# Optimization experiments

Hardware: AMD Instinct MI355X
Metric: run time of the kernel (lower is better)

## Reference

```python
import jax, jax.numpy as jnp
import numpy as np

B, S, D = 4, 512, 256

def setup_inputs() -> dict:
    key = jax.random.key(0)
    ks = jax.random.split(key, 32)
    def w(k, shape, s=0.05):
        return jax.random.normal(k, shape, dtype=jnp.float32) * s
    inp = {
        "img": jax.random.normal(ks[0], (B, S, D), dtype=jnp.float32),
        "audio": jax.random.normal(ks[1], (B, S, D), dtype=jnp.float32),
        "common": jax.random.normal(ks[2], (B, S, D), dtype=jnp.float32),
    }
    names = ["qv", "qa", "kv", "ka", "cc", "w5", "w6", "w7", "w8"]
    for i, n in enumerate(names):
        inp[n + "_w"] = w(ks[3 + 2 * i], (D, D))   # stored [in, out]
        inp[n + "_b"] = w(ks[4 + 2 * i], (D,))
    inp["bil_w"] = w(ks[25], (D, D, D))            # Bilinear weight [out, in1, in2]
    inp["t_o"] = jnp.ones((), dtype=jnp.float32)
    return inp


def reference(img, audio, common,
              qv_w, qv_b, qa_w, qa_b, kv_w, kv_b, ka_w, ka_b, cc_w, cc_b,
              w5_w, w5_b, w6_w, w6_b, w7_w, w7_b, w8_w, w8_b,
              bil_w, t_o):
    dim_k = qv_w.shape[1]
    norm_fact = 1.0 / jnp.sqrt(jnp.asarray(dim_k, dtype=jnp.float32))

    lin = lambda x, w, b: x @ w + b
    # NOTE: faithful to source - softmax first, THEN scaled by norm_fact.
    attn = lambda q, k: jax.nn.softmax(jnp.einsum('bsd,btd->bst', q, k), axis=-1) * norm_fact

    W_q_v = lin(img, qv_w, qv_b)
    W_q_a = lin(audio, qa_w, qa_b)
    w_k_a = lin(audio, ka_w, ka_b)
    W_k_v = lin(img, kv_w, kv_b)
    C_c = lin(common, cc_w, cc_b)

    atten_vv = attn(W_q_v, W_k_v)
    atten_vc = attn(W_q_v, C_c)
    atten_aa = attn(W_q_a, w_k_a)
    atten_ac = attn(W_q_a, C_c)

    vc_common = jnp.einsum('bst,btd->bsd', atten_vc, common)
    ac_common = jnp.einsum('bst,btd->bsd', atten_ac, common)

    common_feat_v = (1.0 + lin(vc_common, w5_w, w5_b)) * jnp.einsum('bst,btd->bsd', atten_vv, img) + lin(vc_common, w6_w, w6_b)
    common_feat_a = (1.0 + lin(ac_common, w7_w, w7_b)) * jnp.einsum('bst,btd->bsd', atten_aa, audio) + lin(ac_common, w8_w, w8_b)

    # Bilinear: out[b,s,k] = v[b,s,:] @ W[k] @ a[b,s,:]
    atten_m = jnp.einsum('bsi,kij,bsj->bsk', common_feat_v, bil_w, common_feat_a)
    j_o = jax.nn.sigmoid(atten_m)
    Z_k_o = t_o * j_o * img + (1.0 - j_o) * audio
    return (Z_k_o + img, Z_k_o + audio)
```

## Files before the change

kernel.cpp:

```cpp
#include <hip/hip_runtime.h>
#include <hip/hip_bf16.h>

typedef unsigned short ushortT;
typedef __bf16 bf16x8 __attribute__((ext_vector_type(8)));
typedef float f32x4 __attribute__((ext_vector_type(4)));
typedef ushortT ush8 __attribute__((ext_vector_type(8)));
typedef ushortT ush4 __attribute__((ext_vector_type(4)));

#define MFMA16(a, b, c) __builtin_amdgcn_mfma_f32_16x16x32_bf16((a), (b), (c), 0, 0, 0)

__device__ __forceinline__ ushortT f2b(float f) {
  __hip_bfloat16 h = __float2bfloat16(f);
  return __builtin_bit_cast(ushortT, h);
}
__device__ __forceinline__ float b2f(ushortT u) {
  __hip_bfloat16 h = __builtin_bit_cast(__hip_bfloat16, u);
  return __bfloat162float(h);
}

__device__ __forceinline__ void async16(const void* g, void* l) {
  __builtin_amdgcn_global_load_lds((const __attribute__((address_space(1))) unsigned int*)g,
                                   (__attribute__((address_space(3))) unsigned int*)l, 16, 0, 0);
}

#define ACT_E 524288
#define WD_E  65536

#define OFF_ACT16   0u
#define OFF_ACTT16  3145728u
#define OFF_W16T    6291456u
#define OFF_PROJ16  7471104u
#define OFF_P16     12713984u
#define OFF_VC16    21102592u
#define OFF_AC16    22151168u
#define OFF_PVV32   23199744u
#define OFF_PVA32   25296896u
#define OFF_PART    0u
#define OFF_BIL16   33554432u
#define OFF_CFV16   67108864u
#define OFF_CFA16   68157440u

__global__ void k_cvt_acts(const float* __restrict__ img, const float* __restrict__ aud,
                           const float* __restrict__ com, ushortT* __restrict__ dst) {
  int i4 = blockIdx.x * 256 + threadIdx.x;
#pragma unroll
  for (int q = 0; q < 4; q++) {
    int idx4 = i4 + q * 98304;
    int flat = idx4 * 4;
    const float* src;
    int off;
    if (flat < 524288)        { src = img; off = flat; }
    else if (flat < 1048576)  { src = aud; off = flat - 524288; }
    else                      { src = com; off = flat - 1048576; }
    float4 v = *(const float4*)(src + off);
    ush4 u = { f2b(v.x), f2b(v.y), f2b(v.z), f2b(v.w) };
    *(ush4*)(dst + idx4 * 4) = u;
  }
}

__global__ void k_cvt_bil(const float* __restrict__ bil, ushortT* __restrict__ dst) {
  int i4 = blockIdx.x * 256 + threadIdx.x;
#pragma unroll
  for (int q = 0; q < 8; q++) {
    int idx4 = i4 + q * 524288;
    float4 v = *(const float4*)(bil + idx4 * 4);
    ush4 u = { f2b(v.x), f2b(v.y), f2b(v.z), f2b(v.w) };
    *(ush4*)(dst + idx4 * 4) = u;
  }
}

__global__ void k_transpose(const float* __restrict__ img, const float* __restrict__ aud,
                            const float* __restrict__ com,
                            const float* w0, const float* w1, const float* w2,
                            const float* w3, const float* w4, const float* w5,
                            const float* w6, const float* w7, const float* w8,
                            ushortT* __restrict__ actT, ushortT* __restrict__ wT) {
  __shared__ ushortT tl[64][72];
  int tid = threadIdx.x;
  int bx = blockIdx.x;
  const float* src;
  ushortT* dst;
  int R, C, r0, c0;
  if (bx < 384) {
    int inst = bx >> 5, tile = bx & 31;
    int act = inst >> 2, bb = inst & 3;
    src = (act == 0 ? img : (act == 1 ? aud : com)) + bb * 131072;
    dst = actT + act * 524288 + bb * 131072;
    R = 512; C = 256;
    r0 = (tile >> 2) * 64; c0 = (tile & 3) * 64;
  } else {
    int bw = bx - 384;
    int w = bw >> 4, tile = bw & 15;
    const float* s;
    switch (w) {
      case 0: s = w0; break; case 1: s = w1; break; case 2: s = w2; break;
      case 3: s = w3; break; case 4: s = w4; break; case 5: s = w5; break;
      case 6: s = w6; break; case 7: s = w7; break; default: s = w8; break;
    }
    src = s;
    dst = wT + w * 65536;
    R = 256; C = 256;
    r0 = (tile >> 2) * 64; c0 = (tile & 3) * 64;
  }
#pragma unroll
  for (int q = 0; q < 4; q++) {
    int rr = q * 16 + (tid >> 4);
    int cs = (tid & 15) * 4;
    float4 v = *(const float4*)(src + (r0 + rr) * C + c0 + cs);
    tl[rr][cs + 0] = f2b(v.x);
    tl[rr][cs + 1] = f2b(v.y);
    tl[rr][cs + 2] = f2b(v.z);
    tl[rr][cs + 3] = f2b(v.w);
  }
  __syncthreads();
#pragma unroll
  for (int q = 0; q < 4; q++) {
    int cc = q * 16 + (tid >> 4);
    int rs = (tid & 15) * 4;
    ush4 u = { tl[rs + 0][cc], tl[rs + 1][cc], tl[rs + 2][cc], tl[rs + 3][cc] };
    *(ush4*)(dst + (c0 + cc) * R + r0 + rs) = u;
  }
}

__global__ __launch_bounds__(512) void k_linear5(
    const ushortT* __restrict__ act16, const ushortT* __restrict__ wT,
    const float* __restrict__ b0, const float* __restrict__ b1,
    const float* __restrict__ b2, const float* __restrict__ b3,
    const float* __restrict__ b4, ushortT* __restrict__ proj16) {
  __shared__ ushortT Al[4][32][8];
  __shared__ ushortT Bl[4][256][8];
  const int tid = threadIdx.x, l = tid & 63, w = tid >> 6;
  const int bx = blockIdx.x;
  const int op = bx >> 6, sblk = bx & 63;
  const int s0 = sblk * 32;
  const int xsel = (op == 4) ? 2 : (op & 1);
  const ushortT* X = act16 + xsel * ACT_E;
  const ushortT* W = wT + op * WD_E;
  const float* bias = op == 0 ? b0 : op == 1 ? b1 : op == 2 ? b2 : op == 3 ? b3 : b4;
  ushortT* out = proj16 + op * ACT_E;

  f32x4 acc[2][2] = {};
  ush8 ra, rb[2];
  int a_row = tid >> 2, a_seg = tid & 3;

  auto sload = [&](int k0) {
    if (tid < 128) ra = *(const ush8*)(X + (s0 + a_row) * 256 + k0 + a_seg * 8);
#pragma unroll
    for (int q = 0; q < 2; q++) {
      int slot = tid + q * 512;
      rb[q] = *(const ush8*)(W + (slot >> 2) * 256 + k0 + (slot & 3) * 8);
    }
  };
  auto swrite = [&]() {
    if (tid < 128) *(ush8*)(&Al[a_seg][a_row][0]) = ra;
#pragma unroll
    for (int q = 0; q < 2; q++) {
      int slot = tid + q * 512;
      *(ush8*)(&Bl[slot & 3][slot >> 2][0]) = rb[q];
    }
  };

  sload(0); swrite(); __syncthreads();
  for (int s = 0; s < 8; s++) {
    if (s < 7) sload((s + 1) * 32);
    int ks = l >> 4;
    bf16x8 a[2], bb[2];
#pragma unroll
    for (int m = 0; m < 2; m++) a[m] = *(const bf16x8*)(&Al[ks][m * 16 + (l & 15)][0]);
#pragma unroll
    for (int n = 0; n < 2; n++) bb[n] = *(const bf16x8*)(&Bl[ks][w * 32 + n * 16 + (l & 15)][0]);
#pragma unroll
    for (int m = 0; m < 2; m++)
#pragma unroll
      for (int n = 0; n < 2; n++) acc[m][n] = MFMA16(a[m], bb[n], acc[m][n]);
    if (s == 7) break;
    __syncthreads();
    swrite();
    __syncthreads();
  }
#pragma unroll
  for (int m = 0; m < 2; m++)
#pragma unroll
    for (int n = 0; n < 2; n++)
#pragma unroll
      for (int r = 0; r < 4; r++) {
        int row = s0 + m * 16 + (l >> 4) * 4 + r;
        int col = w * 32 + n * 16 + (l & 15);
        out[row * 256 + col] = f2b(acc[m][n][r] + bias[col]);
      }
}

__global__ __launch_bounds__(512) void k_attn(const ushortT* __restrict__ proj16,
                                              ushortT* __restrict__ P16) {
  __shared__ ushortT Ql[8][4][32][8];
  __shared__ ushortT Kl[4][512][8];
  __shared__ float red[32][8];
  const int tid = threadIdx.x, l = tid & 63, w = tid >> 6;
  const int bx = blockIdx.x;
  const int p = bx >> 6, b = (bx >> 4) & 3, sblk = bx & 15;
  const int s0 = sblk * 32;
  const int qsel = (p < 2) ? 0 : 1;
  const int ksel = (p == 0) ? 2 : (p == 2) ? 3 : 4;
  const ushortT* Q = proj16 + qsel * ACT_E + b * 131072;
  const ushortT* K = proj16 + ksel * ACT_E + b * 131072;
  ushortT* P = P16 + p * 1048576 + b * 262144;

#pragma unroll
  for (int q = 0; q < 2; q++) {
    int slot = tid + q * 512;
    int row = slot >> 5, seg = slot & 31;
    ush8 v = *(const ush8*)(Q + (s0 + row) * 256 + seg * 8);
    *(ush8*)(&Ql[seg >> 2][seg & 3][row][0]) = v;
  }

  f32x4 acc[2][4] = {};
  ush8 rk[4];
  auto kload = [&](int d0) {
#pragma unroll
    for (int q = 0; q < 4; q++) {
      int slot = tid + q * 512;
      rk[q] = *(const ush8*)(K + (slot >> 2) * 256 + d0 + (slot & 3) * 8);
    }
  };
  auto kwrite = [&]() {
#pragma unroll
    for (int q = 0; q < 4; q++) {
      int slot = tid + q * 512;
      *(ush8*)(&Kl[slot & 3][slot >> 2][0]) = rk[q];
    }
  };

  kload(0); kwrite(); __syncthreads();
  for (int s = 0; s < 8; s++) {
    if (s < 7) kload((s + 1) * 32);
    int ks = l >> 4;
    bf16x8 a[2], bb[4];
#pragma unroll
    for (int m = 0; m < 2; m++) a[m] = *(const bf16x8*)(&Ql[s][ks][m * 16 + (l & 15)][0]);
#pragma unroll
    for (int n = 0; n < 4; n++) bb[n] = *(const bf16x8*)(&Kl[ks][w * 64 + n * 16 + (l & 15)][0]);
#pragma unroll
    for (int m = 0; m < 2; m++)
#pragma unroll
      for (int n = 0; n < 4; n++) acc[m][n] = MFMA16(a[m], bb[n], acc[m][n]);
    if (s == 7) break;
    __syncthreads();
    kwrite();
    __syncthreads();
  }

  float gmax[2][4];
#pragma unroll
  for (int m = 0; m < 2; m++)
#pragma unroll
    for (int r = 0; r < 4; r++) {
      float v = fmaxf(fmaxf(acc[m][0][r], acc[m][1][r]), fmaxf(acc[m][2][r], acc[m][3][r]));
#pragma unroll
      for (int off = 1; off < 16; off <<= 1) v = fmaxf(v, __shfl_xor(v, off, 16));
      if ((l & 15) == 0) red[m * 16 + (l >> 4) * 4 + r][w] = v;
    }
  __syncthreads();
#pragma unroll
  for (int m = 0; m < 2; m++)
#pragma unroll
    for (int r = 0; r < 4; r++) {
      int sr = m * 16 + (l >> 4) * 4 + r;
      float g = red[sr][0];
#pragma unroll
      for (int ww = 1; ww < 8; ww++) g = fmaxf(g, red[sr][ww]);
      gmax[m][r] = g;
    }
  __syncthreads();
#pragma unroll
  for (int m = 0; m < 2; m++)
#pragma unroll
    for (int r = 0; r < 4; r++) {
      float ssum = 0.f;
#pragma unroll
      for (int n = 0; n < 4; n++) {
        float e = __expf(acc[m][n][r] - gmax[m][r]);
        acc[m][n][r] = e;
        ssum += e;
      }
#pragma unroll
      for (int off = 1; off < 16; off <<= 1) ssum += __shfl_xor(ssum, off, 16);
      if ((l & 15) == 0) red[m * 16 + (l >> 4) * 4 + r][w] = ssum;
    }
  __syncthreads();
#pragma unroll
  for (int m = 0; m < 2; m++)
#pragma unroll
    for (int r = 0; r < 4; r++) {
      int sr = m * 16 + (l >> 4) * 4 + r;
      float tot = 0.f;
#pragma unroll
      for (int ww = 0; ww < 8; ww++) tot += red[sr][ww];
      float sc = 0.0625f / tot;
#pragma unroll
      for (int n = 0; n < 4; n++)
        P[(s0 + sr) * 512 + w * 64 + n * 16 + (l & 15)] = f2b(acc[m][n][r] * sc);
    }
}

__global__ __launch_bounds__(512) void k_pv(const ushortT* __restrict__ P16,
                                            const ushortT* __restrict__ actT,
                                            float* __restrict__ pvv, float* __restrict__ pva,
                                            ushortT* __restrict__ vc16, ushortT* __restrict__ ac16) {
  __shared__ ushortT Al[4][32][8];
  __shared__ ushortT Bl[4][256][8];
  const int tid = threadIdx.x, l = tid & 63, w = tid >> 6;
  const int bx = blockIdx.x;
  const int p = bx >> 6, b = (bx >> 4) & 3, sblk = bx & 15;
  const int s0 = sblk * 32;
  const ushortT* A = P16 + p * 1048576 + b * 262144;
  const int vsel = (p == 0) ? 0 : (p == 2) ? 1 : 2;
  const ushortT* VT = actT + vsel * ACT_E + b * 131072;

  f32x4 acc[2][2] = {};
  ush8 ra, rb[2];
  int a_row = tid >> 2, a_seg = tid & 3;
  auto sload = [&](int t0) {
    if (tid < 128) ra = *(const ush8*)(A + (s0 + a_row) * 512 + t0 + a_seg * 8);
#pragma unroll
    for (int q = 0; q < 2; q++) {
      int slot = tid + q * 512;
      rb[q] = *(const ush8*)(VT + (slot >> 2) * 512 + t0 + (slot & 3) * 8);
    }
  };
  auto swrite = [&]() {
    if (tid < 128) *(ush8*)(&Al[a_seg][a_row][0]) = ra;
#pragma unroll
    for (int q = 0; q < 2; q++) {
      int slot = tid + q * 512;
      *(ush8*)(&Bl[slot & 3][slot >> 2][0]) = rb[q];
    }
  };

  sload(0); swrite(); __syncthreads();
  for (int s = 0; s < 16; s++) {
    if (s < 15) sload((s + 1) * 32);
    int ks = l >> 4;
    bf16x8 a[2], bb[2];
#pragma unroll
    for (int m = 0; m < 2; m++) a[m] = *(const bf16x8*)(&Al[ks][m * 16 + (l & 15)][0]);
#pragma unroll
    for (int n = 0; n < 2; n++) bb[n] = *(const bf16x8*)(&Bl[ks][w * 32 + n * 16 + (l & 15)][0]);
#pragma unroll
    for (int m = 0; m < 2; m++)
#pragma unroll
      for (int n = 0; n < 2; n++) acc[m][n] = MFMA16(a[m], bb[n], acc[m][n]);
    if (s == 15) break;
    __syncthreads();
    swrite();
    __syncthreads();
  }
#pragma unroll
  for (int m = 0; m < 2; m++)
#pragma unroll
    for (int n = 0; n < 2; n++)
#pragma unroll
      for (int r = 0; r < 4; r++) {
        int row = s0 + m * 16 + (l >> 4) * 4 + r;
        int col = w * 32 + n * 16 + (l & 15);
        int gi = (b * 512 + row) * 256 + col;
        float v = acc[m][n][r];
        if (p == 0) pvv[gi] = v;
        else if (p == 1) vc16[gi] = f2b(v);
        else if (p == 2) pva[gi] = v;
        else ac16[gi] = f2b(v);
      }
}

__global__ __launch_bounds__(512) void k_lin4c(
    const ushortT* __restrict__ vc16, const ushortT* __restrict__ ac16,
    const ushortT* __restrict__ wT,
    const float* __restrict__ w5b, const float* __restrict__ w6b,
    const float* __restrict__ w7b, const float* __restrict__ w8b,
    const float* __restrict__ pvv, const float* __restrict__ pva,
    ushortT* __restrict__ cfv, ushortT* __restrict__ cfa) {
  __shared__ ushortT Al[4][32][8];
  __shared__ ushortT B1[4][256][8];
  __shared__ ushortT B2[4][256][8];
  const int tid = threadIdx.x, l = tid & 63, w = tid >> 6;
  const int bx = blockIdx.x;
  const int side = bx >> 6, sblk = bx & 63;
  const int s0 = sblk * 32;
  const ushortT* A = side ? ac16 : vc16;
  const ushortT* W1 = wT + (side ? 7 : 5) * WD_E;
  const ushortT* W2 = wT + (side ? 8 : 6) * WD_E;
  const float* bb1 = side ? w7b : w5b;
  const float* bb2 = side ? w8b : w6b;
  const float* pv = side ? pva : pvv;
  ushortT* out = side ? cfa : cfv;

  f32x4 acc1[2][2] = {}, acc2[2][2] = {};
  ush8 ra, rb1[2], rb2[2];
  int a_row = tid >> 2, a_seg = tid & 3;
  auto sload = [&](int k0) {
    if (tid < 128) ra = *(const ush8*)(A + (s0 + a_row) * 256 + k0 + a_seg * 8);
#pragma unroll
    for (int q = 0; q < 2; q++) {
      int slot = tid + q * 512;
      rb1[q] = *(const ush8*)(W1 + (slot >> 2) * 256 + k0 + (slot & 3) * 8);
      rb2[q] = *(const ush8*)(W2 + (slot >> 2) * 256 + k0 + (slot & 3) * 8);
    }
  };
  auto swrite = [&]() {
    if (tid < 128) *(ush8*)(&Al[a_seg][a_row][0]) = ra;
#pragma unroll
    for (int q = 0; q < 2; q++) {
      int slot = tid + q * 512;
      *(ush8*)(&B1[slot & 3][slot >> 2][0]) = rb1[q];
      *(ush8*)(&B2[slot & 3][slot >> 2][0]) = rb2[q];
    }
  };

  sload(0); swrite(); __syncthreads();
  for (int s = 0; s < 8; s++) {
    if (s < 7) sload((s + 1) * 32);
    int ks = l >> 4;
    bf16x8 a[2], x1[2], x2[2];
#pragma unroll
    for (int m = 0; m < 2; m++) a[m] = *(const bf16x8*)(&Al[ks][m * 16 + (l & 15)][0]);
#pragma unroll
    for (int n = 0; n < 2; n++) {
      x1[n] = *(const bf16x8*)(&B1[ks][w * 32 + n * 16 + (l & 15)][0]);
      x2[n] = *(const bf16x8*)(&B2[ks][w * 32 + n * 16 + (l & 15)][0]);
    }
#pragma unroll
    for (int m = 0; m < 2; m++)
#pragma unroll
      for (int n = 0; n < 2; n++) {
        acc1[m][n] = MFMA16(a[m], x1[n], acc1[m][n]);
        acc2[m][n] = MFMA16(a[m], x2[n], acc2[m][n]);
      }
    if (s == 7) break;
    __syncthreads();
    swrite();
    __syncthreads();
  }
#pragma unroll
  for (int m = 0; m < 2; m++)
#pragma unroll
    for (int n = 0; n < 2; n++)
#pragma unroll
      for (int r = 0; r < 4; r++) {
        int row = s0 + m * 16 + (l >> 4) * 4 + r;
        int col = w * 32 + n * 16 + (l & 15);
        int gi = row * 256 + col;
        float u1 = acc1[m][n][r] + bb1[col];
        float u2 = acc2[m][n][r] + bb2[col];
        out[gi] = f2b((1.f + u1) * pv[gi] + u2);
      }
}

__global__ __launch_bounds__(256, 2) void k_bilinear3(
    const ushortT* __restrict__ cfa, const ushortT* __restrict__ cfv,
    const ushortT* __restrict__ W, float* __restrict__ part) {
  __shared__ char arena[57344];
  const int tid = threadIdx.x, l = tid & 63, w = tid >> 6;
  const int bx = blockIdx.x;
  const int ic = bx >> 5;
  const int mb = (bx >> 1) & 15;
  const int nb = bx & 1;
  const int r0 = mb * 128;
  const int ko0 = nb * 128;
  const int wr = w >> 1, wc = w & 1;

  float* cfvl = (float*)(arena + 49152);
  {
    int row = tid >> 1, seg = tid & 1;
    ush8 v = *(const ush8*)(cfv + (r0 + row) * 256 + ic * 16 + seg * 8);
    float* d = cfvl + row * 16 + seg * 8;
#pragma unroll
    for (int q = 0; q < 8; q++) d[q] = b2f(v[q]);
  }
  __syncthreads();

  int aP0 = tid * 16, aP1 = (tid + 256) * 16;
  int aL0 = aP0 ^ (((aP0 >> 7) & 7) << 4);
  int aL1 = aP1 ^ (((aP1 >> 7) & 7) << 4);
  const ushortT* gA0 = cfa + (r0 + (aL0 >> 6)) * 256 + ((aL0 >> 4) & 3) * 8;
  const ushortT* gA1 = cfa + (r0 + (aL1 >> 6)) * 256 + ((aL1 >> 4) & 3) * 8;
  const ushortT* gB0 = W + (ko0 + (aL0 >> 6)) * 65536 + ic * 4096 + ((aL0 >> 4) & 3) * 8;
  const ushortT* gB1 = W + (ko0 + (aL1 >> 6)) * 65536 + ic * 4096 + ((aL1 >> 4) & 3) * 8;

  int aoff[4], boff[4];
#pragma unroll
  for (int m = 0; m < 4; m++) {
    int row = wr * 64 + m * 16 + (l & 15);
    int byte = row * 64 + (l >> 4) * 16;
    aoff[m] = byte ^ (((byte >> 7) & 7) << 4);
  }
#pragma unroll
  for (int n = 0; n < 4; n++) {
    int row = wc * 64 + n * 16 + (l & 15);
    int byte = row * 64 + (l >> 4) * 16;
    boff[n] = byte ^ (((byte >> 7) & 7) << 4);
  }

  f32x4 macc[4][4] = {};
  f32x4 acci[4][4] = {};

  {
    char* Ab = arena;  char* Bb = arena + 24576;
    async16(gA0 + 0, Ab + aP0);  async16(gA1 + 0, Ab + aP1);
    async16(gB0 + 0, Bb + aP0);  async16(gB1 + 0, Bb + aP1);
    Ab += 8192; Bb += 8192;
    async16(gA0 + 32, Ab + aP0); async16(gA1 + 32, Ab + aP1);
    async16(gB0 + 32, Bb + aP0); async16(gB1 + 32, Bb + aP1);
  }

  int bi = 0, si = 2;
  for (int t = 0; t < 128; t++) {
    if (t < 126) asm volatile("s_waitcnt vmcnt(4)" ::: "memory");
    else         asm volatile("s_waitcnt vmcnt(0)" ::: "memory");
    __builtin_amdgcn_s_barrier();

    char* Ab = arena + bi * 8192;
    char* Bb = arena + 24576 + bi * 8192;
    bf16x8 af[4], bf[4];
#pragma unroll
    for (int m = 0; m < 4; m++) af[m] = *(const bf16x8*)(Ab + aoff[m]);
#pragma unroll
    for (int n = 0; n < 4; n++) bf[n] = *(const bf16x8*)(Bb + boff[n]);
#pragma unroll
    for (int m = 0; m < 4; m++)
#pragma unroll
      for (int n = 0; n < 4; n++) acci[m][n] = MFMA16(af[m], bf[n], acci[m][n]);

    if ((t & 7) == 7) {
      int il = t >> 3;
#pragma unroll
      for (int m = 0; m < 4; m++) {
        int rbase = wr * 64 + m * 16 + ((l >> 4) << 2);
        float c0 = cfvl[(rbase + 0) * 16 + il];
        float c1 = cfvl[(rbase + 1) * 16 + il];
        float c2 = cfvl[(rbase + 2) * 16 + il];
        float c3 = cfvl[(rbase + 3) * 16 + il];
#pragma unroll
        for (int n = 0; n < 4; n++) {
          macc[m][n][0] += c0 * acci[m][n][0];
          macc[m][n][1] += c1 * acci[m][n][1];
          macc[m][n][2] += c2 * acci[m][n][2];
          macc[m][n][3] += c3 * acci[m][n][3];
          acci[m][n] = (f32x4){0.f, 0.f, 0.f, 0.f};
        }
      }
    }

    if (t < 126) {
      char* An = arena + si * 8192;
      char* Bn = arena + 24576 + si * 8192;
      int ts = t + 2;
      int js = (ts & 7) * 32;
      async16(gA0 + js, An + aP0);
      async16(gA1 + js, An + aP1);
      async16(gB0 + ts * 32, Bn + aP0);
      async16(gB1 + ts * 32, Bn + aP1);
    }
    bi = (bi == 2) ? 0 : bi + 1;
    si = (si == 2) ? 0 : si + 1;
  }

  float* dst = part + ic * 524288 + r0 * 256 + ko0;
#pragma unroll
  for (int m = 0; m < 4; m++)
#pragma unroll
    for (int n = 0; n < 4; n++)
#pragma unroll
      for (int r = 0; r < 4; r++)
        dst[(wr * 64 + m * 16 + ((l >> 4) << 2) + r) * 256 + wc * 64 + n * 16 + (l & 15)] =
            macc[m][n][r];
}

__global__ void k_final2(const float* __restrict__ part, const float* __restrict__ img,
                         const float* __restrict__ aud, const float* __restrict__ t_o,
                         float* __restrict__ out0, float* __restrict__ out1) {
  int i = blockIdx.x * 256 + threadIdx.x;
  float t = t_o[0];
  float4 m = {0.f, 0.f, 0.f, 0.f};
#pragma unroll
  for (int ic = 0; ic < 16; ic++) {
    float4 p = ((const float4*)(part + ic * 524288))[i];
    m.x += p.x; m.y += p.y; m.z += p.z; m.w += p.w;
  }
  float4 a = ((const float4*)img)[i];
  float4 u = ((const float4*)aud)[i];
  float4 o0, o1;
  {
    float j = 1.f / (1.f + __expf(-m.x)); float Z = t * j * a.x + (1.f - j) * u.x;
    o0.x = Z + a.x; o1.x = Z + u.x;
  }
  {
    float j = 1.f / (1.f + __expf(-m.y)); float Z = t * j * a.y + (1.f - j) * u.y;
    o0.y = Z + a.y; o1.y = Z + u.y;
  }
  {
    float j = 1.f / (1.f + __expf(-m.z)); float Z = t * j * a.z + (1.f - j) * u.z;
    o0.z = Z + a.z; o1.z = Z + u.z;
  }
  {
    float j = 1.f / (1.f + __expf(-m.w)); float Z = t * j * a.w + (1.f - j) * u.w;
    o0.w = Z + a.w; o1.w = Z + u.w;
  }
  ((float4*)out0)[i] = o0;
  ((float4*)out1)[i] = o1;
}

extern "C" void kernel_launch(void* const* d_in, const int* in_sizes, int n_in,
                              void* d_out, int out_size, void* d_ws, size_t ws_size,
                              hipStream_t stream) {
  const float* img   = (const float*)d_in[0];
  const float* aud   = (const float*)d_in[1];
  const float* com   = (const float*)d_in[2];
  const float* qv_w  = (const float*)d_in[3];
  const float* qv_b  = (const float*)d_in[4];
  const float* qa_w  = (const float*)d_in[5];
  const float* qa_b  = (const float*)d_in[6];
  const float* kv_w  = (const float*)d_in[7];
  const float* kv_b  = (const float*)d_in[8];
  const float* ka_w  = (const float*)d_in[9];
  const float* ka_b  = (const float*)d_in[10];
  const float* cc_w  = (const float*)d_in[11];
  const float* cc_b  = (const float*)d_in[12];
  const float* w5_w  = (const float*)d_in[13];
  const float* w5_b  = (const float*)d_in[14];
  const float* w6_w  = (const float*)d_in[15];
  const float* w6_b  = (const float*)d_in[16];
  const float* w7_w  = (const float*)d_in[17];
  const float* w7_b  = (const float*)d_in[18];
  const float* w8_w  = (const float*)d_in[19];
  const float* w8_b  = (const float*)d_in[20];
  const float* bil_w = (const float*)d_in[21];
  const float* t_o   = (const float*)d_in[22];
  float* out = (float*)d_out;

  char* ws = (char*)d_ws;
  ushortT* act16  = (ushortT*)(ws + OFF_ACT16);
  ushortT* actT16 = (ushortT*)(ws + OFF_ACTT16);
  ushortT* w16t   = (ushortT*)(ws + OFF_W16T);
  ushortT* proj16 = (ushortT*)(ws + OFF_PROJ16);
  ushortT* P16    = (ushortT*)(ws + OFF_P16);
  ushortT* vc16   = (ushortT*)(ws + OFF_VC16);
  ushortT* ac16   = (ushortT*)(ws + OFF_AC16);
  float*   pvv32  = (float*)(ws + OFF_PVV32);
  float*   pva32  = (float*)(ws + OFF_PVA32);
  float*   part   = (float*)(ws + OFF_PART);
  ushortT* bil16  = (ushortT*)(ws + OFF_BIL16);
  ushortT* cfv16  = (ushortT*)(ws + OFF_CFV16);
  ushortT* cfa16  = (ushortT*)(ws + OFF_CFA16);

  k_cvt_acts<<<384, 256, 0, stream>>>(img, aud, com, act16);
  k_cvt_bil<<<2048, 256, 0, stream>>>(bil_w, bil16);
  k_transpose<<<528, 256, 0, stream>>>(img, aud, com, qv_w, qa_w, kv_w, ka_w, cc_w,
                                       w5_w, w6_w, w7_w, w8_w, actT16, w16t);
  k_linear5<<<320, 512, 0, stream>>>(act16, w16t, qv_b, qa_b, kv_b, ka_b, cc_b, proj16);
  k_attn<<<256, 512, 0, stream>>>(proj16, P16);
  k_pv<<<256, 512, 0, stream>>>(P16, actT16, pvv32, pva32, vc16, ac16);
  k_lin4c<<<128, 512, 0, stream>>>(vc16, ac16, w16t, w5_b, w6_b, w7_b, w8_b,
                                   pvv32, pva32, cfv16, cfa16);
  k_bilinear3<<<512, 256, 0, stream>>>(cfa16, cfv16, bil16, part);
  k_final2<<<512, 256, 0, stream>>>(part, img, aud, t_o, out, out + 524288);
}
```

Before: 160.0 us.

## Restructure bilinear GEMM to K=64 double-buffered stages with XCD-aware block remap

The bilinear kernel now loads 64-wide K tiles (128-byte rows) into two 32KB LDS buffers instead of three 32-wide buffers. It issues the next stage's async loads after the first half's LDS reads and raises wave priority around the MFMA blocks. It also remaps block indices so blocks landing on the same XCD share W slices, aiming for better L2 reuse. This halves barrier/waitcnt count per K but waits vmcnt(0) each iteration, reducing prefetch depth, and raises LDS use to ~73KB which may limit occupancy to 2 blocks/CU.

```diff
diff --git a/kernel.cpp b/kernel.cpp
--- a/kernel.cpp
+++ b/kernel.cpp
@@ -454,83 +454,113 @@
       }
 }
 
-__global__ __launch_bounds__(256, 2) void k_bilinear3(
+__global__ __launch_bounds__(256, 2) void k_bilinear4(
     const ushortT* __restrict__ cfa, const ushortT* __restrict__ cfv,
     const ushortT* __restrict__ W, float* __restrict__ part) {
-  __shared__ char arena[57344];
+  __shared__ char arena[73728];
   const int tid = threadIdx.x, l = tid & 63, w = tid >> 6;
-  const int bx = blockIdx.x;
-  const int ic = bx >> 5;
-  const int mb = (bx >> 1) & 15;
-  const int nb = bx & 1;
+  const int d = blockIdx.x;
+  const int L = (d & 7) * 64 + (d >> 3);
+  const int ic = L >> 5;
+  const int nb = (L >> 4) & 1;
+  const int mb = L & 15;
   const int r0 = mb * 128;
   const int ko0 = nb * 128;
   const int wr = w >> 1, wc = w & 1;
 
-  float* cfvl = (float*)(arena + 49152);
+  float* cfvl = (float*)(arena + 65536);
   {
     int row = tid >> 1, seg = tid & 1;
     ush8 v = *(const ush8*)(cfv + (r0 + row) * 256 + ic * 16 + seg * 8);
-    float* d = cfvl + row * 16 + seg * 8;
-#pragma unroll
-    for (int q = 0; q < 8; q++) d[q] = b2f(v[q]);
+    float* dptr = cfvl + row * 16 + seg * 8;
+#pragma unroll
+    for (int q = 0; q < 8; q++) dptr[q] = b2f(v[q]);
   }
   __syncthreads();
 
-  int aP0 = tid * 16, aP1 = (tid + 256) * 16;
-  int aL0 = aP0 ^ (((aP0 >> 7) & 7) << 4);
-  int aL1 = aP1 ^ (((aP1 >> 7) & 7) << 4);
-  const ushortT* gA0 = cfa + (r0 + (aL0 >> 6)) * 256 + ((aL0 >> 4) & 3) * 8;
-  const ushortT* gA1 = cfa + (r0 + (aL1 >> 6)) * 256 + ((aL1 >> 4) & 3) * 8;
-  const ushortT* gB0 = W + (ko0 + (aL0 >> 6)) * 65536 + ic * 4096 + ((aL0 >> 4) & 3) * 8;
-  const ushortT* gB1 = W + (ko0 + (aL1 >> 6)) * 65536 + ic * 4096 + ((aL1 >> 4) & 3) * 8;
-
-  int aoff[4], boff[4];
+  const char* gA[4];
+  const char* gB[4];
+#pragma unroll
+  for (int s = 0; s < 4; s++) {
+    int p = (tid + s * 256) * 16;
+    int lg = p ^ (((p >> 7) & 7) << 4);
+    int row = lg >> 7, colb = lg & 127;
+    gA[s] = (const char*)cfa + (size_t)(r0 + row) * 512 + colb;
+    gB[s] = (const char*)W + (size_t)(ko0 + row) * 131072 + (size_t)ic * 8192 + colb;
+  }
+
+  int aoff0[4], aoff1[4], boff0[4], boff1[4];
 #pragma unroll
   for (int m = 0; m < 4; m++) {
     int row = wr * 64 + m * 16 + (l & 15);
-    int byte = row * 64 + (l >> 4) * 16;
-    aoff[m] = byte ^ (((byte >> 7) & 7) << 4);
+    int b0 = row * 128 + (l >> 4) * 16;
+    int msk = (row & 7) << 4;
+    aoff0[m] = b0 ^ msk;
+    aoff1[m] = (b0 + 64) ^ msk;
   }
 #pragma unroll
   for (int n = 0; n < 4; n++) {
     int row = wc * 64 + n * 16 + (l & 15);
-    int byte = row * 64 + (l >> 4) * 16;
-    boff[n] = byte ^ (((byte >> 7) & 7) << 4);
+    int b0 = row * 128 + (l >> 4) * 16;
+    int msk = (row & 7) << 4;
+    boff0[n] = b0 ^ msk;
+    boff1[n] = (b0 + 64) ^ msk;
   }
 
   f32x4 macc[4][4] = {};
   f32x4 acci[4][4] = {};
 
-  {
-    char* Ab = arena;  char* Bb = arena + 24576;
-    async16(gA0 + 0, Ab + aP0);  async16(gA1 + 0, Ab + aP1);
-    async16(gB0 + 0, Bb + aP0);  async16(gB1 + 0, Bb + aP1);
-    Ab += 8192; Bb += 8192;
-    async16(gA0 + 32, Ab + aP0); async16(gA1 + 32, Ab + aP1);
-    async16(gB0 + 32, Bb + aP0); async16(gB1 + 32, Bb + aP1);
-  }
-
-  int bi = 0, si = 2;
-  for (int t = 0; t < 128; t++) {
-    if (t < 126) asm volatile("s_waitcnt vmcnt(4)" ::: "memory");
-    else         asm volatile("s_waitcnt vmcnt(0)" ::: "memory");
+  auto stage = [&](int t, char* bufbase) {
+    int ja = (t & 3) << 7;
+    int jb = t << 7;
+#pragma unroll
+    for (int s = 0; s < 4; s++)
+      async16(gA[s] + ja, bufbase + (tid + s * 256) * 16);
+#pragma unroll
+    for (int s = 0; s < 4; s++)
+      async16(gB[s] + jb, bufbase + 16384 + (tid + s * 256) * 16);
+  };
+
+  stage(0, arena);
+
+  int buf = 0;
+  for (int t = 0; t < 64; t++) {
+    asm volatile("s_waitcnt vmcnt(0)" ::: "memory");
     __builtin_amdgcn_s_barrier();
 
-    char* Ab = arena + bi * 8192;
-    char* Bb = arena + 24576 + bi * 8192;
-    bf16x8 af[4], bf[4];
-#pragma unroll
-    for (int m = 0; m < 4; m++) af[m] = *(const bf16x8*)(Ab + aoff[m]);
-#pragma unroll
-    for (int n = 0; n < 4; n++) bf[n] = *(const bf16x8*)(Bb + boff[n]);
+    char* Ab = arena + buf * 32768;
+    char* Bb = Ab + 16384;
+
+    bf16x8 a0[4], b0v[4];
+#pragma unroll
+    for (int m = 0; m < 4; m++) a0[m] = *(const bf16x8*)(Ab + aoff0[m]);
+#pragma unroll
+    for (int n = 0; n < 4; n++) b0v[n] = *(const bf16x8*)(Bb + boff0[n]);
+
+    if (t < 63) stage(t + 1, arena + (buf ^ 1) * 32768);
+
+    __builtin_amdgcn_s_setprio(1);
 #pragma unroll
     for (int m = 0; m < 4; m++)
 #pragma unroll
-      for (int n = 0; n < 4; n++) acci[m][n] = MFMA16(af[m], bf[n], acci[m][n]);
-
-    if ((t & 7) == 7) {
-      int il = t >> 3;
+      for (int n = 0; n < 4; n++) acci[m][n] = MFMA16(a0[m], b0v[n], acci[m][n]);
+    __builtin_amdgcn_s_setprio(0);
+
+    bf16x8 a1[4], b1v[4];
+#pragma unroll
+    for (int m = 0; m < 4; m++) a1[m] = *(const bf16x8*)(Ab + aoff1[m]);
+#pragma unroll
+    for (int n = 0; n < 4; n++) b1v[n] = *(const bf16x8*)(Bb + boff1[n]);
+
+    __builtin_amdgcn_s_setprio(1);
+#pragma unroll
+    for (int m = 0; m < 4; m++)
+#pragma unroll
+      for (int n = 0; n < 4; n++) acci[m][n] = MFMA16(a1[m], b1v[n], acci[m][n]);
+    __builtin_amdgcn_s_setprio(0);
+
+    if ((t & 3) == 3) {
+      int il = t >> 2;
 #pragma unroll
       for (int m = 0; m < 4; m++) {
         int rbase = wr * 64 + m * 16 + ((l >> 4) << 2);
@@ -548,22 +578,10 @@
         }
       }
     }
-
-    if (t < 126) {
-      char* An = arena + si * 8192;
-      char* Bn = arena + 24576 + si * 8192;
-      int ts = t + 2;
-      int js = (ts & 7) * 32;
-      async16(gA0 + js, An + aP0);
-      async16(gA1 + js, An + aP1);
-      async16(gB0 + ts * 32, Bn + aP0);
-      async16(gB1 + ts * 32, Bn + aP1);
-    }
-    bi = (bi == 2) ? 0 : bi + 1;
-    si = (si == 2) ? 0 : si + 1;
-  }
-
-  float* dst = part + ic * 524288 + r0 * 256 + ko0;
+    buf ^= 1;
+  }
+
+  float* dst = part + (size_t)ic * 524288 + (size_t)r0 * 256 + ko0;
 #pragma unroll
   for (int m = 0; m < 4; m++)
 #pragma unroll
@@ -660,6 +678,6 @@
   k_pv<<<256, 512, 0, stream>>>(P16, actT16, pvv32, pva32, vc16, ac16);
   k_lin4c<<<128, 512, 0, stream>>>(vc16, ac16, w16t, w5_b, w6_b, w7_b, w8_b,
                                    pvv32, pva32, cfv16, cfa16);
-  k_bilinear3<<<512, 256, 0, stream>>>(cfa16, cfv16, bil16, part);
+  k_bilinear4<<<512, 256, 0, stream>>>(cfa16, cfv16, bil16, part);
   k_final2<<<512, 256, 0, stream>>>(part, img, aud, t_o, out, out + 524288);
 }
```

Result: faster. 153.3 us (-4.2%).
